# Kernel tuning notes

Measured on AMD Instinct MI355X. Metric: run time of the kernel, lower is better.

Reference implementation:

```python
import jax, jax.numpy as jnp
import numpy as np

B, C, H, W = 2, 14, 128, 128
LOSS_WEIGHT = 0.5  # output = (1 - loss_weight) * sum of per-(bs,cls) log-Hausdorff losses
BIG = 1e6          # 'infinite' 1D distance for columns with no background pixel


def _edt_sq(is_zero):
    """Exact squared Euclidean distance transform of a [H,W] bool map.

    Returns, for every pixel, the squared distance to the nearest True pixel
    of `is_zero` (0 at True pixels). Matches scipy.ndimage.distance_transform_edt
    squared. Two-phase separable brute force (vectorized, no data loops).
    """
    h, w = is_zero.shape
    ii = jnp.arange(h, dtype=jnp.float32)
    absd = jnp.abs(ii[:, None] - ii[None, :])  # [H(i), H(p)] = |i - p|
    # d1[i, q] = min_{p : is_zero[p, q]} |i - p|   (per-column 1D distance)
    d1 = jnp.min(jnp.where(is_zero[None, :, :], absd[:, :, None], BIG), axis=1)  # [H, W]
    jj = jnp.arange(w, dtype=jnp.float32)
    off = (jj[:, None] - jj[None, :]) ** 2  # [W(q), W(j)] = (q - j)^2
    # sq[i, j] = min_q d1[i, q]^2 + (q - j)^2
    return jnp.min(d1[:, :, None] ** 2 + off[None, :, :], axis=1)  # [H, W]


def _distance_field_sq(img):
    """MONAI HausdorffDTLoss.distance_field squared: (edt(fg)+edt(bg))^2.

    fg_dist and bg_dist have disjoint supports, so (fg+bg)^2 = fg^2 + bg^2.
    Zero field if the image is all-foreground or all-background.
    """
    fg = img > 0.5
    field = _edt_sq(~fg) + _edt_sq(fg)
    valid = jnp.any(fg) & jnp.any(~fg)
    return jnp.where(valid, field, 0.0)


def _edge_mask(m):
    """mask XOR binary_erosion(mask): scipy default cross structuring element,
    border_value=0 (borders erode)."""
    p = jnp.pad(m, 1, constant_values=False)
    er = m & p[:-2, 1:-1] & p[2:, 1:-1] & p[1:-1, :-2] & p[1:-1, 2:]
    return m & ~er


def _pair_loss(stud_logit, seg_s, seg_t, teach_pred):
    # stud_logit: [H,W] float logits of this class; seg_s/seg_t: [H,W] bool
    # class masks; teach_pred: [H,W] teacher argmax labels (int)
    es = _edge_mask(seg_s).astype(stud_logit.dtype)
    et = _edge_mask(seg_t)
    pred = es * stud_logit                                      # edges * logits
    targ = jnp.where(et, teach_pred.astype(stud_logit.dtype), 0.0)  # edges * labels
    pred_dt2 = jax.lax.stop_gradient(_distance_field_sq(pred))  # MONAI detaches dt
    targ_dt2 = jax.lax.stop_gradient(_distance_field_sq(targ))
    hd = jnp.mean((pred - targ) ** 2 * (pred_dt2 + targ_dt2))   # alpha = 2
    return jnp.log(hd + 1.0)                                    # LogHausdorffDTLoss


def reference(logits_student, logits_teacher):
    ps = jnp.argmax(logits_student, axis=1)  # softmax is monotone -> argmax of logits
    pt = jnp.argmax(logits_teacher, axis=1)
    cls = jnp.arange(1, C)                   # classes 1..C-1 (background skipped)
    n = B * (C - 1)
    seg_s = (ps[:, None] == cls[None, :, None, None]).reshape(n, H, W)
    seg_t = (pt[:, None] == cls[None, :, None, None]).reshape(n, H, W)
    stud = logits_student[:, 1:].reshape(n, H, W)
    pt_rep = jnp.broadcast_to(pt[:, None], (B, C - 1, H, W)).reshape(n, H, W)
    losses = jax.vmap(_pair_loss)(stud, seg_s, seg_t, pt_rep)
    return (1.0 - LOSS_WEIGHT) * jnp.sum(losses)


def setup_inputs() -> dict:
    key = jax.random.key(0)
    k1, k2 = jax.random.split(key)
    return {
        "logits_student": jax.random.normal(k1, (B, C, H, W), dtype=jnp.float32),
        "logits_teacher": jax.random.normal(k2, (B, C, H, W), dtype=jnp.float32),
    }
```

## Files before the change

kernel.cpp:

```cpp
#include <hip/hip_runtime.h>
#include <math.h>
#include <limits.h>

#define HH 128
#define WW 128
#define HW (HH*WW)
#define BB 2
#define CC 14
#define NPAIR 26
#define RPB 8
#define NBLK (NPAIR * (HH / RPB))

typedef unsigned long long u64;


__device__ inline int nbd(u64 lo, u64 hi, int i) {
    int up = 255, down = 255;
    u64 slo, shi;
    if (i == 0)      { slo = lo; shi = hi; }
    else if (i < 64) { slo = (lo >> i) | (hi << (64 - i)); shi = hi >> i; }
    else             { slo = hi >> (i - 64); shi = 0ULL; }
    if (slo)      up = __builtin_ctzll(slo);
    else if (shi) up = 64 + __builtin_ctzll(shi);
    int s = 127 - i;
    u64 llo, lhi;
    if (s == 0)      { llo = lo; lhi = hi; }
    else if (s < 64) { lhi = (hi << s) | (lo >> (64 - s)); llo = lo << s; }
    else             { lhi = lo << (s - 64); llo = 0ULL; }
    if (lhi)      down = __builtin_clzll(lhi);
    else if (llo) down = 64 + __builtin_clzll(llo);
    return min(up, down);
}

__global__ void k_argmax(const float* __restrict__ Ls, const float* __restrict__ Lt,
                         unsigned char* __restrict__ ps, unsigned char* __restrict__ pt,
                         float* __restrict__ sums, int* __restrict__ done) {
    if (blockIdx.x == 0) {
        if (threadIdx.x < NPAIR) sums[threadIdx.x] = 0.0f;
        if (threadIdx.x == 0) *done = 0;
    }
    int tid = blockIdx.x * blockDim.x + threadIdx.x;
    const int total4 = BB * HW / 4;
    if (tid >= 2 * total4) return;
    const float* L; unsigned char* dst; int p4;
    if (tid < total4) { L = Ls; dst = ps; p4 = tid; }
    else              { L = Lt; dst = pt; p4 = tid - total4; }
    int b = p4 / (HW / 4);
    int q4 = p4 - b * (HW / 4);
    const float4* base = (const float4*)(L + (size_t)b * CC * HW) + q4;
    float4 best = base[0];
    uchar4 bi = make_uchar4(0, 0, 0, 0);
#pragma unroll
    for (int c = 1; c < CC; ++c) {
        float4 v = base[(size_t)c * (HW / 4)];
        if (v.x > best.x) { best.x = v.x; bi.x = (unsigned char)c; }
        if (v.y > best.y) { best.y = v.y; bi.y = (unsigned char)c; }
        if (v.z > best.z) { best.z = v.z; bi.z = (unsigned char)c; }
        if (v.w > best.w) { best.w = v.w; bi.w = (unsigned char)c; }
    }
    ((uchar4*)dst)[b * (HW / 4) + q4] = bi;
}

__device__ inline u64 asm64(unsigned int (*p)[WW], int k0, int j) {
    return (u64)p[k0][j] | ((u64)p[k0 + 1][j] << 16)
         | ((u64)p[k0 + 2][j] << 32) | ((u64)p[k0 + 3][j] << 48);
}

__global__ __launch_bounds__(1024) void k_C(
        const unsigned char* __restrict__ ps, const unsigned char* __restrict__ pt,
        const float* __restrict__ Ls,
        float* __restrict__ sums, int* __restrict__ done, float* __restrict__ out) {
    int n = blockIdx.x >> 4;
    int t = blockIdx.x & 15;
    int tid = threadIdx.x;
    int k = tid >> 7;
    int j = tid & (WW - 1);
    int b = n / (CC - 1), c = 1 + (n - b * (CC - 1));
    const unsigned char* P = ps + b * HW;
    const unsigned char* T = pt + b * HW;
    const float* Lp = Ls + (size_t)(b * CC + c) * HW;

    int i = t * RPB + k;
    float lv = Lp[i * WW + j];

    unsigned int s16 = 0, t16 = 0, h16 = 0;
    int i0 = k << 4;
#pragma unroll
    for (int r = 0; r < 16; ++r) {
        int off = (i0 + r) * WW + j;
        if (P[off] == c)              s16 |= 1u << r;
        if (T[off] == c)              t16 |= 1u << r;
        if (Lp[off] > 0.5f)           h16 |= 1u << r;
    }
    __shared__ unsigned int pS[8][WW], pT[8][WW], pH[8][WW];
    pS[k][j] = s16; pT[k][j] = t16; pH[k][j] = h16;
    __syncthreads();

    __shared__ ulonglong2 colFP[WW], colET[WW], colES[WW];
    __shared__ int sfl[2];
    if (tid < WW) {
        u64 ms0 = asm64(pS, 0, j), ms1 = asm64(pS, 4, j);
        u64 mt0 = asm64(pT, 0, j), mt1 = asm64(pT, 4, j);
        u64 hi0 = asm64(pH, 0, j), hi1 = asm64(pH, 4, j);
        u64 Lsx = 0, Lsy = 0, Ltx = 0, Lty = 0, Rsx = 0, Rsy = 0, Rtx = 0, Rty = 0;
        if (j > 0)      { Lsx = asm64(pS, 0, j - 1); Lsy = asm64(pS, 4, j - 1);
                          Ltx = asm64(pT, 0, j - 1); Lty = asm64(pT, 4, j - 1); }
        if (j < WW - 1) { Rsx = asm64(pS, 0, j + 1); Rsy = asm64(pS, 4, j + 1);
                          Rtx = asm64(pT, 0, j + 1); Rty = asm64(pT, 4, j + 1); }

        u64 U0 = ms0 << 1, U1 = (ms1 << 1) | (ms0 >> 63);
        u64 D0 = (ms0 >> 1) | (ms1 << 63), D1 = ms1 >> 1;
        u64 er0 = ms0 & U0 & D0 & Lsx & Rsx;
        u64 er1 = ms1 & U1 & D1 & Lsy & Rsy;
        u64 es0 = ms0 & ~er0, es1 = ms1 & ~er1;

        u64 Ut0 = mt0 << 1, Ut1 = (mt1 << 1) | (mt0 >> 63);
        u64 Dt0 = (mt0 >> 1) | (mt1 << 63), Dt1 = mt1 >> 1;
        u64 ert0 = mt0 & Ut0 & Dt0 & Ltx & Rtx;
        u64 ert1 = mt1 & Ut1 & Dt1 & Lty & Rty;
        u64 et0 = mt0 & ~ert0, et1 = mt1 & ~ert1;

        u64 fp0 = es0 & hi0, fp1 = es1 & hi1;

        colFP[j] = make_ulonglong2(fp0, fp1);
        colET[j] = make_ulonglong2(et0, et1);
        colES[j] = make_ulonglong2(es0, es1);

        u64 bFgP = __ballot((fp0 | fp1) != 0ull);
        u64 bBgP = __ballot((fp0 & fp1) != ~0ull);
        u64 bFgT = __ballot((et0 | et1) != 0ull);
        u64 bBgT = __ballot((et0 & et1) != ~0ull);
        if ((tid & 63) == 0) {
            sfl[tid >> 6] = (bFgP ? 1 : 0) | (bBgP ? 2 : 0)
                          | (bFgT ? 4 : 0) | (bBgT ? 8 : 0);
        }
    }
    __syncthreads();

    ulonglong2 mP = colFP[j];
    ulonglong2 mT = colET[j];
    ulonglong2 eS = colES[j];
    int f = sfl[0] | sfl[1];
    bool aP = (f & 3) == 3, aT = (f & 12) == 12;

    int dP  = nbd(mP.x, mP.y, i);
    int dPb = nbd(~mP.x, ~mP.y, i);
    int dT  = nbd(mT.x, mT.y, i);
    int dTb = nbd(~mT.x, ~mT.y, i);

    __shared__ uchar4 sq[RPB][WW];
    sq[k][j] = make_uchar4((unsigned char)dP, (unsigned char)dPb,
                           (unsigned char)dT, (unsigned char)dTb);
    __syncthreads();

    int bP = dP * dP, bPb = dPb * dPb, bT = dT * dT, bTb = dTb * dTb;
    int need = 0;
    if (aP) need = max(bP, bPb);
    if (aT) need = max(need, max(bT, bTb));
    for (int rad = 1; rad < WW; ++rad) {
        int rr = rad * rad;
        if (rr >= need) break;
        if (j >= rad) {
            uchar4 s = sq[k][j - rad];
            bP  = min(bP,  (int)s.x * s.x + rr); bPb = min(bPb, (int)s.y * s.y + rr);
            bT  = min(bT,  (int)s.z * s.z + rr); bTb = min(bTb, (int)s.w * s.w + rr);
        }
        if (j + rad < WW) {
            uchar4 s = sq[k][j + rad];
            bP  = min(bP,  (int)s.x * s.x + rr); bPb = min(bPb, (int)s.y * s.y + rr);
            bT  = min(bT,  (int)s.z * s.z + rr); bTb = min(bTb, (int)s.w * s.w + rr);
        }
        need = 0;
        if (aP) need = max(bP, bPb);
        if (aT) need = max(need, max(bT, bTb));
    }

    float fieldP = aP ? (float)(bP + bPb) : 0.0f;
    float fieldT = aT ? (float)(bT + bTb) : 0.0f;

    bool es = ((i < 64 ? (eS.x >> i) : (eS.y >> (i - 64))) & 1ull) != 0;
    bool et = ((i < 64 ? (mT.x >> i) : (mT.y >> (i - 64))) & 1ull) != 0;
    float predv = es ? lv : 0.0f;
    float targv = et ? (float)c : 0.0f;
    float diff = predv - targv;
    float v = diff * diff * (fieldP + fieldT);

    for (int o = 32; o > 0; o >>= 1) v += __shfl_down(v, o);
    __shared__ float wsum[16];
    __shared__ int won;
    int lane = threadIdx.x & 63, w = threadIdx.x >> 6;
    if (lane == 0) wsum[w] = v;
    if (threadIdx.x == 0) won = 0;
    __syncthreads();
    if (threadIdx.x == 0) {
        float tot = 0.0f;
#pragma unroll
        for (int q = 0; q < 16; ++q) tot += wsum[q];
        atomicAdd(&sums[n], tot);
        __threadfence();
        if (atomicAdd(done, 1) == NBLK - 1) won = 1;
    }
    __syncthreads();
    if (won && threadIdx.x < 64) {
        float vv = 0.0f;
        if (threadIdx.x < NPAIR) {
            float hd = atomicAdd(&sums[threadIdx.x], 0.0f) * (1.0f / (float)HW);
            vv = logf(hd + 1.0f);
        }
        for (int o = 32; o > 0; o >>= 1) vv += __shfl_down(vv, o);
        if (threadIdx.x == 0) out[0] = 0.5f * vv;
    }
}

extern "C" void kernel_launch(void* const* d_in, const int* in_sizes, int n_in,
                              void* d_out, int out_size, void* d_ws, size_t ws_size,
                              hipStream_t stream) {
    const float* Ls = (const float*)d_in[0];
    const float* Lt = (const float*)d_in[1];
    float* out = (float*)d_out;

    char* w = (char*)d_ws;
    unsigned char* ps   = (unsigned char*)(w);
    unsigned char* pt   = (unsigned char*)(w + 32768);
    float*         sums = (float*)        (w + 65536);
    int*           done = (int*)          (w + 65664);

    k_argmax<<<(2 * BB * HW / 4 + 255) / 256, 256, 0, stream>>>(Ls, Lt, ps, pt, sums, done);
    k_C<<<NBLK, 1024, 0, stream>>>(ps, pt, Ls, sums, done, out);
}
```

Baseline: 72.40 us.

## Fuse argmax and distance-loss kernels with a software grid barrier

Merges the argmax kernel into the main loss kernel. Each of the 416 blocks first computes a slice of the argmax labels, then all blocks meet at a global atomic spin barrier before the distance-transform stage. Counters are now zeroed with a memset. This removes one kernel launch and the gap between kernels, but it relies on all 416 blocks of 1024 threads being resident at once, otherwise the barrier deadlocks, and it adds a spin-wait cost.

```diff
diff --git a/kernel.cpp b/kernel.cpp
--- a/kernel.cpp
+++ b/kernel.cpp
@@ -10,6 +10,8 @@
 #define NPAIR 26
 #define RPB 8
 #define NBLK (NPAIR * (HH / RPB))
+#define NUNIT (2 * BB * HW / 4)
+#define UPB ((NUNIT + NBLK - 1) / NBLK)
 
 typedef unsigned long long u64;
 
@@ -32,47 +34,53 @@
     return min(up, down);
 }
 
-__global__ void k_argmax(const float* __restrict__ Ls, const float* __restrict__ Lt,
-                         unsigned char* __restrict__ ps, unsigned char* __restrict__ pt,
-                         float* __restrict__ sums, int* __restrict__ done) {
-    if (blockIdx.x == 0) {
-        if (threadIdx.x < NPAIR) sums[threadIdx.x] = 0.0f;
-        if (threadIdx.x == 0) *done = 0;
-    }
-    int tid = blockIdx.x * blockDim.x + threadIdx.x;
-    const int total4 = BB * HW / 4;
-    if (tid >= 2 * total4) return;
-    const float* L; unsigned char* dst; int p4;
-    if (tid < total4) { L = Ls; dst = ps; p4 = tid; }
-    else              { L = Lt; dst = pt; p4 = tid - total4; }
-    int b = p4 / (HW / 4);
-    int q4 = p4 - b * (HW / 4);
-    const float4* base = (const float4*)(L + (size_t)b * CC * HW) + q4;
-    float4 best = base[0];
-    uchar4 bi = make_uchar4(0, 0, 0, 0);
-#pragma unroll
-    for (int c = 1; c < CC; ++c) {
-        float4 v = base[(size_t)c * (HW / 4)];
-        if (v.x > best.x) { best.x = v.x; bi.x = (unsigned char)c; }
-        if (v.y > best.y) { best.y = v.y; bi.y = (unsigned char)c; }
-        if (v.z > best.z) { best.z = v.z; bi.z = (unsigned char)c; }
-        if (v.w > best.w) { best.w = v.w; bi.w = (unsigned char)c; }
-    }
-    ((uchar4*)dst)[b * (HW / 4) + q4] = bi;
-}
-
 __device__ inline u64 asm64(unsigned int (*p)[WW], int k0, int j) {
     return (u64)p[k0][j] | ((u64)p[k0 + 1][j] << 16)
          | ((u64)p[k0 + 2][j] << 32) | ((u64)p[k0 + 3][j] << 48);
 }
 
-__global__ __launch_bounds__(1024) void k_C(
-        const unsigned char* __restrict__ ps, const unsigned char* __restrict__ pt,
-        const float* __restrict__ Ls,
-        float* __restrict__ sums, int* __restrict__ done, float* __restrict__ out) {
+__global__ __launch_bounds__(1024) void k_all(
+        const float* __restrict__ Ls, const float* __restrict__ Lt,
+        unsigned char* __restrict__ ps, unsigned char* __restrict__ pt,
+        float* __restrict__ sums, int* __restrict__ done, int* __restrict__ bar,
+        float* __restrict__ out) {
+    int tid = threadIdx.x;
+
+    if (tid < UPB) {
+        int u = blockIdx.x * UPB + tid;
+        if (u < NUNIT) {
+            const float* L; unsigned char* dst;
+            int p4 = u & (NUNIT / 2 - 1);
+            if (u < NUNIT / 2) { L = Ls; dst = ps; }
+            else               { L = Lt; dst = pt; }
+            int b = p4 >> 12;
+            int q4 = p4 & (HW / 4 - 1);
+            const float4* base = (const float4*)(L + (size_t)b * CC * HW) + q4;
+            float4 best = base[0];
+            uchar4 bi = make_uchar4(0, 0, 0, 0);
+#pragma unroll
+            for (int c = 1; c < CC; ++c) {
+                float4 v = base[(size_t)c * (HW / 4)];
+                if (v.x > best.x) { best.x = v.x; bi.x = (unsigned char)c; }
+                if (v.y > best.y) { best.y = v.y; bi.y = (unsigned char)c; }
+                if (v.z > best.z) { best.z = v.z; bi.z = (unsigned char)c; }
+                if (v.w > best.w) { best.w = v.w; bi.w = (unsigned char)c; }
+            }
+            ((uchar4*)dst)[b * (HW / 4) + q4] = bi;
+        }
+    }
+
+    __syncthreads();
+    if (tid == 0) {
+        __threadfence();
+        atomicAdd(bar, 1);
+        while (atomicAdd(bar, 0) < NBLK) { }
+        __threadfence();
+    }
+    __syncthreads();
+
     int n = blockIdx.x >> 4;
     int t = blockIdx.x & 15;
-    int tid = threadIdx.x;
     int k = tid >> 7;
     int j = tid & (WW - 1);
     int b = n / (CC - 1), c = 1 + (n - b * (CC - 1));
@@ -188,11 +196,11 @@
     for (int o = 32; o > 0; o >>= 1) v += __shfl_down(v, o);
     __shared__ float wsum[16];
     __shared__ int won;
-    int lane = threadIdx.x & 63, w = threadIdx.x >> 6;
+    int lane = tid & 63, w = tid >> 6;
     if (lane == 0) wsum[w] = v;
-    if (threadIdx.x == 0) won = 0;
-    __syncthreads();
-    if (threadIdx.x == 0) {
+    if (tid == 0) won = 0;
+    __syncthreads();
+    if (tid == 0) {
         float tot = 0.0f;
 #pragma unroll
         for (int q = 0; q < 16; ++q) tot += wsum[q];
@@ -201,14 +209,14 @@
         if (atomicAdd(done, 1) == NBLK - 1) won = 1;
     }
     __syncthreads();
-    if (won && threadIdx.x < 64) {
+    if (won && tid < 64) {
         float vv = 0.0f;
-        if (threadIdx.x < NPAIR) {
-            float hd = atomicAdd(&sums[threadIdx.x], 0.0f) * (1.0f / (float)HW);
+        if (tid < NPAIR) {
+            float hd = atomicAdd(&sums[tid], 0.0f) * (1.0f / (float)HW);
             vv = logf(hd + 1.0f);
         }
         for (int o = 32; o > 0; o >>= 1) vv += __shfl_down(vv, o);
-        if (threadIdx.x == 0) out[0] = 0.5f * vv;
+        if (tid == 0) out[0] = 0.5f * vv;
     }
 }
 
@@ -224,7 +232,8 @@
     unsigned char* pt   = (unsigned char*)(w + 32768);
     float*         sums = (float*)        (w + 65536);
     int*           done = (int*)          (w + 65664);
-
-    k_argmax<<<(2 * BB * HW / 4 + 255) / 256, 256, 0, stream>>>(Ls, Lt, ps, pt, sums, done);
-    k_C<<<NBLK, 1024, 0, stream>>>(ps, pt, Ls, sums, done, out);
-}
+    int*           bar  = (int*)          (w + 65668);
+
+    hipMemsetAsync(w + 65536, 0, 136, stream);
+    k_all<<<NBLK, 1024, 0, stream>>>(Ls, Lt, ps, pt, sums, done, bar, out);
+}
```

After: 102.2 us. +41.1%, slower.

## Pack student/teacher labels into nibbles and precompute logit threshold bitmask

Applied to the files above, without the earlier changes.

The argmax kernel now handles student and teacher in the same thread. It packs both labels into one byte (4 bits each) and also records a 13-bit mask of which student class logits exceed 0.5. The main kernel then reads one label byte and one 16-bit mask per pixel instead of two label bytes plus a float logit from the class plane, which cuts its global traffic across 16 rows per thread. The trade-off is half as many threads in the argmax kernel, each doing twice the loads.

```diff
diff --git a/kernel.cpp b/kernel.cpp
--- a/kernel.cpp
+++ b/kernel.cpp
@@ -33,32 +33,45 @@
 }
 
 __global__ void k_argmax(const float* __restrict__ Ls, const float* __restrict__ Lt,
-                         unsigned char* __restrict__ ps, unsigned char* __restrict__ pt,
+                         unsigned char* __restrict__ lab, unsigned short* __restrict__ hb,
                          float* __restrict__ sums, int* __restrict__ done) {
     if (blockIdx.x == 0) {
         if (threadIdx.x < NPAIR) sums[threadIdx.x] = 0.0f;
         if (threadIdx.x == 0) *done = 0;
     }
-    int tid = blockIdx.x * blockDim.x + threadIdx.x;
-    const int total4 = BB * HW / 4;
-    if (tid >= 2 * total4) return;
-    const float* L; unsigned char* dst; int p4;
-    if (tid < total4) { L = Ls; dst = ps; p4 = tid; }
-    else              { L = Lt; dst = pt; p4 = tid - total4; }
-    int b = p4 / (HW / 4);
-    int q4 = p4 - b * (HW / 4);
-    const float4* base = (const float4*)(L + (size_t)b * CC * HW) + q4;
-    float4 best = base[0];
-    uchar4 bi = make_uchar4(0, 0, 0, 0);
+    int p4 = blockIdx.x * blockDim.x + threadIdx.x;
+    if (p4 >= BB * HW / 4) return;
+    int b = p4 >> 12;
+    int q4 = p4 & (HW / 4 - 1);
+    const float4* bs = (const float4*)(Ls + (size_t)b * CC * HW) + q4;
+    const float4* bt = (const float4*)(Lt + (size_t)b * CC * HW) + q4;
+    float4 mS = bs[0], mT = bt[0];
+    uchar4 iS = make_uchar4(0, 0, 0, 0), iT = make_uchar4(0, 0, 0, 0);
+    ushort4 hm = make_ushort4(0, 0, 0, 0);
 #pragma unroll
     for (int c = 1; c < CC; ++c) {
-        float4 v = base[(size_t)c * (HW / 4)];
-        if (v.x > best.x) { best.x = v.x; bi.x = (unsigned char)c; }
-        if (v.y > best.y) { best.y = v.y; bi.y = (unsigned char)c; }
-        if (v.z > best.z) { best.z = v.z; bi.z = (unsigned char)c; }
-        if (v.w > best.w) { best.w = v.w; bi.w = (unsigned char)c; }
-    }
-    ((uchar4*)dst)[b * (HW / 4) + q4] = bi;
+        float4 v = bs[(size_t)c * (HW / 4)];
+        if (v.x > mS.x) { mS.x = v.x; iS.x = (unsigned char)c; }
+        if (v.y > mS.y) { mS.y = v.y; iS.y = (unsigned char)c; }
+        if (v.z > mS.z) { mS.z = v.z; iS.z = (unsigned char)c; }
+        if (v.w > mS.w) { mS.w = v.w; iS.w = (unsigned char)c; }
+        unsigned short bit = (unsigned short)(1u << (c - 1));
+        if (v.x > 0.5f) hm.x |= bit;
+        if (v.y > 0.5f) hm.y |= bit;
+        if (v.z > 0.5f) hm.z |= bit;
+        if (v.w > 0.5f) hm.w |= bit;
+        float4 u = bt[(size_t)c * (HW / 4)];
+        if (u.x > mT.x) { mT.x = u.x; iT.x = (unsigned char)c; }
+        if (u.y > mT.y) { mT.y = u.y; iT.y = (unsigned char)c; }
+        if (u.z > mT.z) { mT.z = u.z; iT.z = (unsigned char)c; }
+        if (u.w > mT.w) { mT.w = u.w; iT.w = (unsigned char)c; }
+    }
+    uchar4 pk = make_uchar4((unsigned char)(iS.x | (iT.x << 4)),
+                            (unsigned char)(iS.y | (iT.y << 4)),
+                            (unsigned char)(iS.z | (iT.z << 4)),
+                            (unsigned char)(iS.w | (iT.w << 4)));
+    ((uchar4*)lab)[b * (HW / 4) + q4] = pk;
+    ((ushort4*)hb)[b * (HW / 4) + q4] = hm;
 }
 
 __device__ inline u64 asm64(unsigned int (*p)[WW], int k0, int j) {
@@ -67,7 +80,7 @@
 }
 
 __global__ __launch_bounds__(1024) void k_C(
-        const unsigned char* __restrict__ ps, const unsigned char* __restrict__ pt,
+        const unsigned char* __restrict__ lab, const unsigned short* __restrict__ hb,
         const float* __restrict__ Ls,
         float* __restrict__ sums, int* __restrict__ done, float* __restrict__ out) {
     int n = blockIdx.x >> 4;
@@ -76,8 +89,8 @@
     int k = tid >> 7;
     int j = tid & (WW - 1);
     int b = n / (CC - 1), c = 1 + (n - b * (CC - 1));
-    const unsigned char* P = ps + b * HW;
-    const unsigned char* T = pt + b * HW;
+    const unsigned char*  LB = lab + b * HW;
+    const unsigned short* HB = hb + b * HW;
     const float* Lp = Ls + (size_t)(b * CC + c) * HW;
 
     int i = t * RPB + k;
@@ -85,12 +98,14 @@
 
     unsigned int s16 = 0, t16 = 0, h16 = 0;
     int i0 = k << 4;
+    unsigned int hbit = 1u << (c - 1);
 #pragma unroll
     for (int r = 0; r < 16; ++r) {
         int off = (i0 + r) * WW + j;
-        if (P[off] == c)              s16 |= 1u << r;
-        if (T[off] == c)              t16 |= 1u << r;
-        if (Lp[off] > 0.5f)           h16 |= 1u << r;
+        unsigned int lbv = LB[off];
+        if ((lbv & 15u) == (unsigned)c)  s16 |= 1u << r;
+        if ((lbv >> 4)  == (unsigned)c)  t16 |= 1u << r;
+        if (HB[off] & hbit)              h16 |= 1u << r;
     }
     __shared__ unsigned int pS[8][WW], pT[8][WW], pH[8][WW];
     pS[k][j] = s16; pT[k][j] = t16; pH[k][j] = h16;
@@ -188,11 +203,11 @@
     for (int o = 32; o > 0; o >>= 1) v += __shfl_down(v, o);
     __shared__ float wsum[16];
     __shared__ int won;
-    int lane = threadIdx.x & 63, w = threadIdx.x >> 6;
+    int lane = tid & 63, w = tid >> 6;
     if (lane == 0) wsum[w] = v;
-    if (threadIdx.x == 0) won = 0;
-    __syncthreads();
-    if (threadIdx.x == 0) {
+    if (tid == 0) won = 0;
+    __syncthreads();
+    if (tid == 0) {
         float tot = 0.0f;
 #pragma unroll
         for (int q = 0; q < 16; ++q) tot += wsum[q];
@@ -201,14 +216,14 @@
         if (atomicAdd(done, 1) == NBLK - 1) won = 1;
     }
     __syncthreads();
-    if (won && threadIdx.x < 64) {
+    if (won && tid < 64) {
         float vv = 0.0f;
-        if (threadIdx.x < NPAIR) {
-            float hd = atomicAdd(&sums[threadIdx.x], 0.0f) * (1.0f / (float)HW);
+        if (tid < NPAIR) {
+            float hd = atomicAdd(&sums[tid], 0.0f) * (1.0f / (float)HW);
             vv = logf(hd + 1.0f);
         }
         for (int o = 32; o > 0; o >>= 1) vv += __shfl_down(vv, o);
-        if (threadIdx.x == 0) out[0] = 0.5f * vv;
+        if (tid == 0) out[0] = 0.5f * vv;
     }
 }
 
@@ -220,11 +235,11 @@
     float* out = (float*)d_out;
 
     char* w = (char*)d_ws;
-    unsigned char* ps   = (unsigned char*)(w);
-    unsigned char* pt   = (unsigned char*)(w + 32768);
-    float*         sums = (float*)        (w + 65536);
-    int*           done = (int*)          (w + 65664);
-
-    k_argmax<<<(2 * BB * HW / 4 + 255) / 256, 256, 0, stream>>>(Ls, Lt, ps, pt, sums, done);
-    k_C<<<NBLK, 1024, 0, stream>>>(ps, pt, Ls, sums, done, out);
-}
+    unsigned char*  lab  = (unsigned char*) (w);
+    unsigned short* hbm  = (unsigned short*)(w + 32768);
+    float*          sums = (float*)         (w + 98304);
+    int*            done = (int*)           (w + 98432);
+
+    k_argmax<<<BB * HW / 4 / 256, 256, 0, stream>>>(Ls, Lt, lab, hbm, sums, done);
+    k_C<<<NBLK, 1024, 0, stream>>>(lab, hbm, Ls, sums, done, out);
+}
```

Result: no change. 71.75 us (-0.9%).
